# Performance work log

Hardware: AMD Instinct MI355X
Metric: run time of the kernel (lower is better)

## Reference

```python
import jax, jax.numpy as jnp
import numpy as np

B, S, D, T = 8, 4096, 512, 8  # batch, seq (dim), d_model, nheads


def _sinusoidal_pe(dim, d_model):
    # matches torch: pe[:,0::2]=sin(pos*div), pe[:,1::2]=cos(pos*div)
    pos = jnp.arange(dim, dtype=jnp.float32)[:, None]
    div = jnp.exp(jnp.arange(0, d_model, 2, dtype=jnp.float32) * (-(np.log(10000.0) / d_model)))
    ang = pos * div  # [dim, d_model//2]
    return jnp.stack([jnp.sin(ang), jnp.cos(ang)], axis=-1).reshape(dim, d_model)


def setup_inputs() -> dict:
    key = jax.random.key(0)
    ks = jax.random.split(key, 7)
    sc = 1.0 / np.sqrt(D)
    return {
        "x": jax.random.normal(ks[0], (B, S, D), dtype=jnp.float32),
        "Wk": jax.random.normal(ks[1], (T, D, D), dtype=jnp.float32) * sc,
        "bk": jax.random.normal(ks[2], (T, D), dtype=jnp.float32) * sc,
        "Wq": jax.random.normal(ks[3], (T, D, D), dtype=jnp.float32) * sc,
        "bq": jax.random.normal(ks[4], (T, D), dtype=jnp.float32) * sc,
        "Wv": jax.random.normal(ks[5], (T, D, D), dtype=jnp.float32) * sc,
        "bv": jax.random.normal(ks[6], (T, D), dtype=jnp.float32) * sc,
    }


def reference(x, Wk, bk, Wq, bq, Wv, bv):
    b, s, d = x.shape
    t = Wk.shape[0]
    c = s // t  # head chunk length
    x = x + _sinusoidal_pe(s, d)[None]  # PE add
    xh = x.reshape(b, t, c, d)  # 'b (t c) d -> b t c d'
    # torch Linear: y = x @ W^T + b ; W is [out, in]
    k = jnp.einsum('btcd,ted->btce', xh, Wk) + bk[None, :, None, :]
    q = jnp.einsum('btcd,ted->btce', xh, Wq) + bq[None, :, None, :]
    v = jnp.einsum('btcd,ted->btce', xh, Wv) + bv[None, :, None, :]
    # note: k @ q^T (not q @ k^T) and divide by d_model (not sqrt) -- faithful
    scores = jnp.einsum('btid,btjd->btij', k, q) * (1.0 / d)
    attn = jax.nn.softmax(scores, axis=-1)
    out = jnp.einsum('btij,btjd->btid', attn, v)
    return out.reshape(b, s, d)  # concat heads along seq dim
```

## Files before the change

### kernel.cpp

```cpp
#include <hip/hip_runtime.h>
#include <hip/hip_bf16.h>
#include <cstdint>
#include <cstddef>


typedef __bf16 bf16_t;
typedef __bf16 bf16x4 __attribute__((ext_vector_type(4)));
typedef __bf16 bf16x8 __attribute__((ext_vector_type(8)));
typedef float  f32x4  __attribute__((ext_vector_type(4)));

#define GAS __attribute__((address_space(1)))
#define LAS __attribute__((address_space(3)))

__global__ __launch_bounds__(256) void pe_cast_kernel(
    const float* __restrict__ x, bf16_t* __restrict__ xpe, int n4)
{
    const float cexp = -0.017988946039015984f;
    for (int i = blockIdx.x * 256 + threadIdx.x; i < n4; i += gridDim.x * 256) {
        int e0 = i << 2;
        int d  = e0 & 511;
        int s  = (e0 >> 9) & 4095;
        float4 xv = ((const float4*)x)[i];
        float fs = (float)s;
        float a0 = fs * __expf(cexp * (float)d);
        float a1 = fs * __expf(cexp * (float)(d + 2));
        float s0, c0, s1, c1;
        sincosf(a0, &s0, &c0);
        sincosf(a1, &s1, &c1);
        bf16x4 o;
        o[0] = (bf16_t)(xv.x + s0);
        o[1] = (bf16_t)(xv.y + c0);
        o[2] = (bf16_t)(xv.z + s1);
        o[3] = (bf16_t)(xv.w + c1);
        ((bf16x4*)xpe)[i] = o;
    }
}

__global__ __launch_bounds__(256) void cast_w(
    const float* __restrict__ w0, const float* __restrict__ w1, const float* __restrict__ w2,
    bf16_t* __restrict__ o0, bf16_t* __restrict__ o1, bf16_t* __restrict__ o2, int n4)
{
    const float* s = blockIdx.y == 0 ? w0 : (blockIdx.y == 1 ? w1 : w2);
    bf16_t*      o = blockIdx.y == 0 ? o0 : (blockIdx.y == 1 ? o1 : o2);
    for (int i = blockIdx.x * 256 + threadIdx.x; i < n4; i += gridDim.x * 256) {
        float4 v = ((const float4*)s)[i];
        bf16x4 r;
        r[0] = (bf16_t)v.x; r[1] = (bf16_t)v.y; r[2] = (bf16_t)v.z; r[3] = (bf16_t)v.w;
        ((bf16x4*)o)[i] = r;
    }
}

template<int BIAS_MODE, int OUT_BF16>
__global__ __launch_bounds__(256, 2) void gemm_nt(
    const bf16_t* __restrict__ A, const bf16_t* __restrict__ Bm,
    void* __restrict__ C, const float* __restrict__ bias,
    long aStr, long bStr, long cStr, int aByT, int bByT, float scale)
{
    constexpr int LD = 512;
    int bt = blockIdx.y;
    int t  = bt & 7;
    const bf16_t* Ab = A  + (size_t)(aByT ? t : bt) * aStr;
    const bf16_t* Bb = Bm + (size_t)(bByT ? t : bt) * bStr;
    int ti = (blockIdx.x >> 2) << 7;
    int tn = (blockIdx.x & 3) << 7;

    __shared__ bf16_t lds[16384];
    char* ldsA = (char*)&lds[0];
    char* ldsB = (char*)&lds[8192];

    const int tid  = threadIdx.x;
    const int l    = tid & 63;
    const int w    = tid >> 6;
    const int lrow = l >> 3;
    const int hd   = (l & 7) ^ lrow;
    const int wrow = w >> 1, wcol = w & 1;
    const int rA   = l & 15;
    const int hb   = l >> 4;
    const int x7   = l & 7;

    f32x4 acc[4][4] = {};

    for (int k0 = 0; k0 < 512; k0 += 64) {
        __syncthreads();
        #pragma unroll
        for (int p = 0; p < 4; ++p) {
            int c    = w * 4 + p;
            int grow = c * 8 + lrow;
            const bf16_t* srcA = Ab + (size_t)(ti + grow) * LD + k0 + hd * 8;
            const bf16_t* srcB = Bb + (size_t)(tn + grow) * LD + k0 + hd * 8;
            __builtin_amdgcn_global_load_lds((GAS void*)srcA, (LAS void*)(ldsA + c * 1024 + l * 16), 16, 0, 0);
            __builtin_amdgcn_global_load_lds((GAS void*)srcB, (LAS void*)(ldsB + c * 1024 + l * 16), 16, 0, 0);
        }
        __syncthreads();
        #pragma unroll
        for (int kk = 0; kk < 2; ++kk) {
            bf16x8 a[4], b[4];
            #pragma unroll
            for (int m = 0; m < 4; ++m) {
                int off = (wrow * 64 + m * 16 + rA) * 128 + ((((kk << 2) | hb)) ^ x7) * 16;
                a[m] = *(const bf16x8*)(ldsA + off);
            }
            #pragma unroll
            for (int n = 0; n < 4; ++n) {
                int off = (wcol * 64 + n * 16 + rA) * 128 + ((((kk << 2) | hb)) ^ x7) * 16;
                b[n] = *(const bf16x8*)(ldsB + off);
            }
            #pragma unroll
            for (int m = 0; m < 4; ++m)
                #pragma unroll
                for (int n = 0; n < 4; ++n)
                    acc[m][n] = __builtin_amdgcn_mfma_f32_16x16x32_bf16(a[m], b[n], acc[m][n], 0, 0, 0);
        }
    }

    const float* biasT = bias ? bias + t * 512 : bias;
    int r0 = ti + wrow * 64;
    int c0 = tn + wcol * 64;
    #pragma unroll
    for (int m = 0; m < 4; ++m) {
        #pragma unroll
        for (int n = 0; n < 4; ++n) {
            int col = c0 + n * 16 + rA;
            float bc = (BIAS_MODE == 1) ? biasT[col] : 0.0f;
            f32x4 v = acc[m][n];
            #pragma unroll
            for (int r = 0; r < 4; ++r) {
                int row = r0 + m * 16 + hb * 4 + r;
                float val = v[r] * scale + ((BIAS_MODE == 2) ? biasT[row] : bc);
                size_t off = (size_t)bt * cStr + (size_t)row * LD + col;
                if (OUT_BF16) ((bf16_t*)C)[off] = (bf16_t)val;
                else          ((float*)C)[off]  = val;
            }
        }
    }
}

__global__ __launch_bounds__(256) void softmax_rows(
    const float* __restrict__ S, bf16_t* __restrict__ P)
{
    int row = blockIdx.x * 4 + (threadIdx.x >> 6);
    int l   = threadIdx.x & 63;
    const float4* rp = (const float4*)(S + (size_t)row * 512);
    float4 v0 = rp[l];
    float4 v1 = rp[64 + l];
    float m = fmaxf(fmaxf(fmaxf(v0.x, v0.y), fmaxf(v0.z, v0.w)),
                    fmaxf(fmaxf(v1.x, v1.y), fmaxf(v1.z, v1.w)));
    #pragma unroll
    for (int off = 32; off; off >>= 1) m = fmaxf(m, __shfl_xor(m, off, 64));
    float e0 = __expf(v0.x - m), e1 = __expf(v0.y - m), e2 = __expf(v0.z - m), e3 = __expf(v0.w - m);
    float e4 = __expf(v1.x - m), e5 = __expf(v1.y - m), e6 = __expf(v1.z - m), e7 = __expf(v1.w - m);
    float sum = ((e0 + e1) + (e2 + e3)) + ((e4 + e5) + (e6 + e7));
    #pragma unroll
    for (int off = 32; off; off >>= 1) sum += __shfl_xor(sum, off, 64);
    float inv = 1.0f / sum;
    bf16x4 r0, r1;
    r0[0] = (bf16_t)(e0 * inv); r0[1] = (bf16_t)(e1 * inv);
    r0[2] = (bf16_t)(e2 * inv); r0[3] = (bf16_t)(e3 * inv);
    r1[0] = (bf16_t)(e4 * inv); r1[1] = (bf16_t)(e5 * inv);
    r1[2] = (bf16_t)(e6 * inv); r1[3] = (bf16_t)(e7 * inv);
    bf16x4* wp = (bf16x4*)(P + (size_t)row * 512);
    wp[l] = r0; wp[64 + l] = r1;
}

extern "C" void kernel_launch(void* const* d_in, const int* in_sizes, int n_in,
                              void* d_out, int out_size, void* d_ws, size_t ws_size,
                              hipStream_t stream)
{
    const float* x  = (const float*)d_in[0];
    const float* Wk = (const float*)d_in[1];
    const float* bk = (const float*)d_in[2];
    const float* Wq = (const float*)d_in[3];
    const float* bq = (const float*)d_in[4];
    const float* Wv = (const float*)d_in[5];
    const float* bv = (const float*)d_in[6];
    float* out = (float*)d_out;
    char*  ws  = (char*)d_ws;

    bf16_t* k    = (bf16_t*)(ws + 0);
    bf16_t* q    = (bf16_t*)(ws + 33554432);
    bf16_t* vt   = (bf16_t*)(ws + 67108864);
    bf16_t* xpe  = (bf16_t*)(ws + 100663296);
    bf16_t* attn = xpe;
    bf16_t* wkb  = (bf16_t*)(ws + 134217728);
    bf16_t* wqb  = (bf16_t*)(ws + 138412032);
    bf16_t* wvb  = (bf16_t*)(ws + 142606336);
    float* scores = out;

    const long S2 = 262144;

    pe_cast_kernel<<<2048, 256, 0, stream>>>(x, xpe, (8 * 4096 * 512) / 4);
    cast_w<<<dim3(512, 3), 256, 0, stream>>>(Wk, Wq, Wv, wkb, wqb, wvb, (8 * 512 * 512) / 4);

    dim3 gg(16, 64);
    gemm_nt<1, 1><<<gg, 256, 0, stream>>>(xpe, wkb, k, bk, S2, S2, S2, 0, 1, 1.0f);
    gemm_nt<1, 1><<<gg, 256, 0, stream>>>(xpe, wqb, q, bq, S2, S2, S2, 0, 1, 1.0f);
    gemm_nt<2, 1><<<gg, 256, 0, stream>>>(wvb, xpe, vt, bv, S2, S2, S2, 1, 0, 1.0f);
    gemm_nt<0, 0><<<gg, 256, 0, stream>>>(k, q, scores, nullptr, S2, S2, S2, 0, 0, 1.0f / 512.0f);
    softmax_rows<<<8192, 256, 0, stream>>>(scores, attn);
    gemm_nt<0, 0><<<gg, 256, 0, stream>>>(attn, vt, out, nullptr, S2, S2, S2, 0, 0, 1.0f);
}
```

Before: 314.3 us.

## Fuse scores GEMM with softmax, double-buffer GEMM LDS, remap block order and PE compute

A new kernel computes the K·Qᵀ scores for a full 128x512 row tile and applies the softmax in registers, with cross-wave max and sum reductions through LDS. This removes the fp32 scores round trip through global memory and one kernel launch. The generic GEMM now double-buffers its LDS tiles so the next global-to-LDS load overlaps the MFMA work, and it remaps block indices to change cache locality. The PE kernel computes sin/cos once per (s,d) and reuses them across the 8 batches. In exchange, the fused kernel launches only 256 blocks of 512 threads with a large LDS footprint, so occupancy drops.

```diff
diff --git a/kernel.cpp b/kernel.cpp
--- a/kernel.cpp
+++ b/kernel.cpp
@@ -13,26 +13,29 @@
 #define LAS __attribute__((address_space(3)))
 
 __global__ __launch_bounds__(256) void pe_cast_kernel(
-    const float* __restrict__ x, bf16_t* __restrict__ xpe, int n4)
+    const float* __restrict__ x, bf16_t* __restrict__ xpe)
 {
     const float cexp = -0.017988946039015984f;
-    for (int i = blockIdx.x * 256 + threadIdx.x; i < n4; i += gridDim.x * 256) {
-        int e0 = i << 2;
-        int d  = e0 & 511;
-        int s  = (e0 >> 9) & 4095;
-        float4 xv = ((const float4*)x)[i];
-        float fs = (float)s;
-        float a0 = fs * __expf(cexp * (float)d);
-        float a1 = fs * __expf(cexp * (float)(d + 2));
-        float s0, c0, s1, c1;
-        sincosf(a0, &s0, &c0);
-        sincosf(a1, &s1, &c1);
+    int i = blockIdx.x * 256 + threadIdx.x;
+    int d4 = i & 127;
+    int s  = i >> 7;
+    int d  = d4 * 4;
+    float fs = (float)s;
+    float a0 = fs * __expf(cexp * (float)d);
+    float a1 = fs * __expf(cexp * (float)(d + 2));
+    float s0, c0, s1, c1;
+    sincosf(a0, &s0, &c0);
+    sincosf(a1, &s1, &c1);
+    size_t base = (size_t)s * 512 + d;
+    #pragma unroll
+    for (int b = 0; b < 8; ++b) {
+        float4 xv = *(const float4*)(x + (size_t)b * 2097152 + base);
         bf16x4 o;
         o[0] = (bf16_t)(xv.x + s0);
         o[1] = (bf16_t)(xv.y + c0);
         o[2] = (bf16_t)(xv.z + s1);
         o[3] = (bf16_t)(xv.w + c1);
-        ((bf16x4*)xpe)[i] = o;
+        *(bf16x4*)(xpe + (size_t)b * 2097152 + base) = o;
     }
 }
 
@@ -57,16 +60,17 @@
     long aStr, long bStr, long cStr, int aByT, int bByT, float scale)
 {
     constexpr int LD = 512;
-    int bt = blockIdx.y;
+    int L  = blockIdx.y * 16 + blockIdx.x;
+    int wk = (L & 7) * 128 + (L >> 3);
+    int bt = wk >> 4;
+    int tile = wk & 15;
     int t  = bt & 7;
     const bf16_t* Ab = A  + (size_t)(aByT ? t : bt) * aStr;
     const bf16_t* Bb = Bm + (size_t)(bByT ? t : bt) * bStr;
-    int ti = (blockIdx.x >> 2) << 7;
-    int tn = (blockIdx.x & 3) << 7;
-
-    __shared__ bf16_t lds[16384];
-    char* ldsA = (char*)&lds[0];
-    char* ldsB = (char*)&lds[8192];
+    int ti = (tile >> 2) << 7;
+    int tn = (tile & 3) << 7;
+
+    __shared__ __align__(1024) char lds[65536];
 
     const int tid  = threadIdx.x;
     const int l    = tid & 63;
@@ -80,8 +84,9 @@
 
     f32x4 acc[4][4] = {};
 
-    for (int k0 = 0; k0 < 512; k0 += 64) {
-        __syncthreads();
+    auto stage = [&](int buf, int k0) {
+        char* ldsA = lds + buf * 32768;
+        char* ldsB = ldsA + 16384;
         #pragma unroll
         for (int p = 0; p < 4; ++p) {
             int c    = w * 4 + p;
@@ -91,7 +96,14 @@
             __builtin_amdgcn_global_load_lds((GAS void*)srcA, (LAS void*)(ldsA + c * 1024 + l * 16), 16, 0, 0);
             __builtin_amdgcn_global_load_lds((GAS void*)srcB, (LAS void*)(ldsB + c * 1024 + l * 16), 16, 0, 0);
         }
-        __syncthreads();
+    };
+
+    stage(0, 0);
+    __syncthreads();
+    for (int it = 0; it < 8; ++it) {
+        if (it < 7) stage((it + 1) & 1, (it + 1) * 64);
+        const char* ldsA = lds + (it & 1) * 32768;
+        const char* ldsB = ldsA + 16384;
         #pragma unroll
         for (int kk = 0; kk < 2; ++kk) {
             bf16x8 a[4], b[4];
@@ -111,6 +123,7 @@
                 for (int n = 0; n < 4; ++n)
                     acc[m][n] = __builtin_amdgcn_mfma_f32_16x16x32_bf16(a[m], b[n], acc[m][n], 0, 0, 0);
         }
+        __syncthreads();
     }
 
     const float* biasT = bias ? bias + t * 512 : bias;
@@ -135,31 +148,140 @@
     }
 }
 
-__global__ __launch_bounds__(256) void softmax_rows(
-    const float* __restrict__ S, bf16_t* __restrict__ P)
-{
-    int row = blockIdx.x * 4 + (threadIdx.x >> 6);
-    int l   = threadIdx.x & 63;
-    const float4* rp = (const float4*)(S + (size_t)row * 512);
-    float4 v0 = rp[l];
-    float4 v1 = rp[64 + l];
-    float m = fmaxf(fmaxf(fmaxf(v0.x, v0.y), fmaxf(v0.z, v0.w)),
-                    fmaxf(fmaxf(v1.x, v1.y), fmaxf(v1.z, v1.w)));
-    #pragma unroll
-    for (int off = 32; off; off >>= 1) m = fmaxf(m, __shfl_xor(m, off, 64));
-    float e0 = __expf(v0.x - m), e1 = __expf(v0.y - m), e2 = __expf(v0.z - m), e3 = __expf(v0.w - m);
-    float e4 = __expf(v1.x - m), e5 = __expf(v1.y - m), e6 = __expf(v1.z - m), e7 = __expf(v1.w - m);
-    float sum = ((e0 + e1) + (e2 + e3)) + ((e4 + e5) + (e6 + e7));
-    #pragma unroll
-    for (int off = 32; off; off >>= 1) sum += __shfl_xor(sum, off, 64);
-    float inv = 1.0f / sum;
-    bf16x4 r0, r1;
-    r0[0] = (bf16_t)(e0 * inv); r0[1] = (bf16_t)(e1 * inv);
-    r0[2] = (bf16_t)(e2 * inv); r0[3] = (bf16_t)(e3 * inv);
-    r1[0] = (bf16_t)(e4 * inv); r1[1] = (bf16_t)(e5 * inv);
-    r1[2] = (bf16_t)(e6 * inv); r1[3] = (bf16_t)(e7 * inv);
-    bf16x4* wp = (bf16x4*)(P + (size_t)row * 512);
-    wp[l] = r0; wp[64 + l] = r1;
+__global__ __launch_bounds__(512, 2) void scores_softmax(
+    const bf16_t* __restrict__ K, const bf16_t* __restrict__ Q,
+    bf16_t* __restrict__ P)
+{
+    int L  = blockIdx.x;
+    int wk = (L & 7) * 32 + (L >> 3);
+    int bt = wk >> 2;
+    int ti = (wk & 3) << 7;
+    const bf16_t* Kb = K + (size_t)bt * 262144;
+    const bf16_t* Qb = Q + (size_t)bt * 262144;
+
+    __shared__ __align__(1024) char smem[86016];
+    float* smax_p = (float*)(smem + 81920);
+    float* ssum_p = (float*)(smem + 83968);
+
+    const int tid  = threadIdx.x;
+    const int l    = tid & 63;
+    const int wv   = tid >> 6;
+    const int wrow = wv >> 2;
+    const int wcol = wv & 3;
+    const int rA   = l & 15;
+    const int hb   = l >> 4;
+
+    f32x4 acc[4][8] = {};
+
+    auto stage = [&](int buf, int d0) {
+        char* kA = smem + buf * 8192;
+        char* qB = smem + 16384 + buf * 32768;
+        {
+            int row = tid >> 2, slot = tid & 3;
+            const bf16_t* src = Kb + (size_t)(ti + row) * 512 + d0 + (slot ^ (row & 3)) * 8;
+            __builtin_amdgcn_global_load_lds((GAS void*)src, (LAS void*)(kA + tid * 16), 16, 0, 0);
+        }
+        #pragma unroll
+        for (int u = 0; u < 4; ++u) {
+            int q2 = u * 512 + tid;
+            int row = q2 >> 2, slot = q2 & 3;
+            const bf16_t* src = Qb + (size_t)row * 512 + d0 + (slot ^ (row & 3)) * 8;
+            __builtin_amdgcn_global_load_lds((GAS void*)src, (LAS void*)(qB + q2 * 16), 16, 0, 0);
+        }
+    };
+
+    stage(0, 0);
+    __syncthreads();
+    for (int it = 0; it < 16; ++it) {
+        if (it < 15) stage((it + 1) & 1, (it + 1) * 32);
+        const char* kA = smem + (it & 1) * 8192;
+        const char* qB = smem + 16384 + (it & 1) * 32768;
+        bf16x8 a[4], b[8];
+        #pragma unroll
+        for (int m = 0; m < 4; ++m) {
+            int row = wrow * 64 + m * 16 + rA;
+            a[m] = *(const bf16x8*)(kA + row * 64 + (hb ^ (row & 3)) * 16);
+        }
+        #pragma unroll
+        for (int n = 0; n < 8; ++n) {
+            int row = wcol * 128 + n * 16 + rA;
+            b[n] = *(const bf16x8*)(qB + row * 64 + (hb ^ (row & 3)) * 16);
+        }
+        #pragma unroll
+        for (int m = 0; m < 4; ++m)
+            #pragma unroll
+            for (int n = 0; n < 8; ++n)
+                acc[m][n] = __builtin_amdgcn_mfma_f32_16x16x32_bf16(a[m], b[n], acc[m][n], 0, 0, 0);
+        __syncthreads();
+    }
+
+    float red[4][4];
+    #pragma unroll
+    for (int m = 0; m < 4; ++m)
+        #pragma unroll
+        for (int r = 0; r < 4; ++r) {
+            float mx = acc[m][0][r];
+            #pragma unroll
+            for (int n = 1; n < 8; ++n) mx = fmaxf(mx, acc[m][n][r]);
+            #pragma unroll
+            for (int o = 1; o < 16; o <<= 1) mx = fmaxf(mx, __shfl_xor(mx, o, 64));
+            red[m][r] = mx;
+        }
+    if (rA < 4) {
+        #pragma unroll
+        for (int m = 0; m < 4; ++m)
+            smax_p[(wrow * 64 + m * 16 + hb * 4 + rA) * 4 + wcol] = red[m][rA];
+    }
+    __syncthreads();
+    float rstat[4][4];
+    #pragma unroll
+    for (int m = 0; m < 4; ++m)
+        #pragma unroll
+        for (int r = 0; r < 4; ++r) {
+            f32x4 p4 = *(const f32x4*)(smax_p + (wrow * 64 + m * 16 + hb * 4 + r) * 4);
+            rstat[m][r] = fmaxf(fmaxf(p4[0], p4[1]), fmaxf(p4[2], p4[3]));
+        }
+    const float inv512 = 1.0f / 512.0f;
+    #pragma unroll
+    for (int m = 0; m < 4; ++m)
+        #pragma unroll
+        for (int r = 0; r < 4; ++r) {
+            float sum = 0.0f;
+            #pragma unroll
+            for (int n = 0; n < 8; ++n) {
+                float e = __expf((acc[m][n][r] - rstat[m][r]) * inv512);
+                acc[m][n][r] = e;
+                sum += e;
+            }
+            #pragma unroll
+            for (int o = 1; o < 16; o <<= 1) sum += __shfl_xor(sum, o, 64);
+            red[m][r] = sum;
+        }
+    if (rA < 4) {
+        #pragma unroll
+        for (int m = 0; m < 4; ++m)
+            ssum_p[(wrow * 64 + m * 16 + hb * 4 + rA) * 4 + wcol] = red[m][rA];
+    }
+    __syncthreads();
+    #pragma unroll
+    for (int m = 0; m < 4; ++m)
+        #pragma unroll
+        for (int r = 0; r < 4; ++r) {
+            f32x4 p4 = *(const f32x4*)(ssum_p + (wrow * 64 + m * 16 + hb * 4 + r) * 4);
+            rstat[m][r] = 1.0f / (((p4[0] + p4[1]) + (p4[2] + p4[3])));
+        }
+    #pragma unroll
+    for (int m = 0; m < 4; ++m)
+        #pragma unroll
+        for (int n = 0; n < 8; ++n) {
+            int col = wcol * 128 + n * 16 + rA;
+            #pragma unroll
+            for (int r = 0; r < 4; ++r) {
+                int row = ti + wrow * 64 + m * 16 + hb * 4 + r;
+                P[(size_t)bt * 262144 + (size_t)row * 512 + col] =
+                    (bf16_t)(acc[m][n][r] * rstat[m][r]);
+            }
+        }
 }
 
 extern "C" void kernel_launch(void* const* d_in, const int* in_sizes, int n_in,
@@ -184,18 +306,16 @@
     bf16_t* wkb  = (bf16_t*)(ws + 134217728);
     bf16_t* wqb  = (bf16_t*)(ws + 138412032);
     bf16_t* wvb  = (bf16_t*)(ws + 142606336);
-    float* scores = out;
 
     const long S2 = 262144;
 
-    pe_cast_kernel<<<2048, 256, 0, stream>>>(x, xpe, (8 * 4096 * 512) / 4);
+    pe_cast_kernel<<<2048, 256, 0, stream>>>(x, xpe);
     cast_w<<<dim3(512, 3), 256, 0, stream>>>(Wk, Wq, Wv, wkb, wqb, wvb, (8 * 512 * 512) / 4);
 
     dim3 gg(16, 64);
     gemm_nt<1, 1><<<gg, 256, 0, stream>>>(xpe, wkb, k, bk, S2, S2, S2, 0, 1, 1.0f);
     gemm_nt<1, 1><<<gg, 256, 0, stream>>>(xpe, wqb, q, bq, S2, S2, S2, 0, 1, 1.0f);
     gemm_nt<2, 1><<<gg, 256, 0, stream>>>(wvb, xpe, vt, bv, S2, S2, S2, 1, 0, 1.0f);
-    gemm_nt<0, 0><<<gg, 256, 0, stream>>>(k, q, scores, nullptr, S2, S2, S2, 0, 0, 1.0f / 512.0f);
-    softmax_rows<<<8192, 256, 0, stream>>>(scores, attn);
+    scores_softmax<<<256, 512, 0, stream>>>(k, q, attn);
     gemm_nt<0, 0><<<gg, 256, 0, stream>>>(attn, vt, out, nullptr, S2, S2, S2, 0, 0, 1.0f);
 }
```

New measurement: 274.1 us. -12.8%, faster.
